# Kernel tuning notes

Hardware: AMD Instinct MI355X
Metric: run time of the kernel (lower is better)

Reference implementation:

```python
import jax, jax.numpy as jnp
import numpy as np

EPS = 1e-8


def _entropy_1d(p):
    # entropy() helper with input_as_probabilities=True on a 1-D tensor:
    # clamp to EPS, x*log(x), return -sum
    p_ = jnp.maximum(p, EPS)
    return -jnp.sum(p_ * jnp.log(p_))


def setup_inputs() -> dict:
    key = jax.random.key(0)
    k1, k2 = jax.random.split(key)
    b, n = 65536, 512
    anchors = jax.random.normal(k1, (b, n), dtype=jnp.float32)
    neighbors = jax.random.normal(k2, (b, n), dtype=jnp.float32)
    return {"anchors": anchors, "neighbors": neighbors}


def reference(anchors, neighbors):
    entropy_weight = 2.0
    b, n = anchors.shape

    anchors_prob = jax.nn.softmax(anchors, axis=1)      # [b, n]
    positives_prob = jax.nn.softmax(neighbors, axis=1)  # [b, n]

    # bmm of [b,1,n] x [b,n,1] -> row-wise dot product, shape [b]
    similarity = jnp.einsum('bn,bn->b', anchors_prob, positives_prob)

    # BCELoss(similarity, ones) = -mean(log(sim)); torch clamps log at -100
    consistency_loss = -jnp.mean(jnp.maximum(jnp.log(similarity), -100.0))

    lg_sim = jnp.log(similarity)

    entropy_loss = _entropy_1d(jnp.mean(anchors_prob, axis=0))

    # cross/second-order: dot of clamped sim with clamped log-sim
    second_order_loss = jnp.dot(jnp.maximum(similarity, EPS),
                                jnp.maximum(lg_sim, EPS))

    # np.tile(sim, n).reshape(n, b) then view(b, n, 1): equivalent to the
    # flat [b*n] tiled vector reshaped row-major to [b, n]
    tiled_sim = jnp.tile(similarity, n).reshape(b, n)
    third_order_entropy = jnp.einsum('bn,bn->b', anchors_prob, tiled_sim)
    lg_third = jnp.log(third_order_entropy)
    third_order_loss = jnp.dot(jnp.maximum(third_order_entropy, EPS),
                               jnp.maximum(lg_third, EPS)) / n

    third_weight = 0.5 / np.sqrt(n)
    diff_weight = 0.25 / n

    total_loss = (consistency_loss
                  - entropy_weight * entropy_loss
                  + diff_weight * second_order_loss
                  - third_weight * third_order_loss)
    return (total_loss, consistency_loss, entropy_loss,
            second_order_loss, third_order_loss)
```

## Files before the change

### kernel.cpp

```cpp
#include <hip/hip_runtime.h>
#include <math.h>

#define B_ROWS 65536
#define N_COLS 512
#define EPS 1e-8f
#define GRID1 2048


__global__ __launch_bounds__(256) void k_main(
        const float* __restrict__ A, const float* __restrict__ Bn,
        float* __restrict__ sim, float* __restrict__ colsum,
        float* __restrict__ acc) {
    __shared__ float cs[512];
    __shared__ float sred[8];
    const int t    = threadIdx.x;
    const int lane = t & 63;
    const int w    = t >> 6;
    const int s    = blockIdx.x & 127;
    const int kb   = (blockIdx.x >> 7) * 32 + w * 8;

    cs[t] = 0.f; cs[t + 256] = 0.f;

    float cacc[8];
#pragma unroll
    for (int k = 0; k < 8; ++k) cacc[k] = 0.f;
    float accLog = 0.f, accSim = 0.f;

#pragma unroll
    for (int batch = 0; batch < 2; ++batch) {
        int rows[4];
        float4 a0[4], a1[4], b0[4], b1[4];
#pragma unroll
        for (int q = 0; q < 4; ++q) {
            rows[q] = s + 128 * (kb + batch * 4 + q);
            const float* a = A  + (size_t)rows[q] * N_COLS;
            const float* b = Bn + (size_t)rows[q] * N_COLS;
            a0[q] = *(const float4*)(a + lane * 4);
            a1[q] = *(const float4*)(a + 256 + lane * 4);
            b0[q] = *(const float4*)(b + lane * 4);
            b1[q] = *(const float4*)(b + 256 + lane * 4);
        }
        float ea[4][8], sa[4], sb[4], dp[4];
#pragma unroll
        for (int q = 0; q < 4; ++q) {
            float av[8] = {a0[q].x, a0[q].y, a0[q].z, a0[q].w,
                           a1[q].x, a1[q].y, a1[q].z, a1[q].w};
            float bv[8] = {b0[q].x, b0[q].y, b0[q].z, b0[q].w,
                           b1[q].x, b1[q].y, b1[q].z, b1[q].w};
            float sA = 0.f, sB = 0.f, d = 0.f;
#pragma unroll
            for (int k = 0; k < 8; ++k) {
                float e = __expf(av[k]);
                float f = __expf(bv[k]);
                ea[q][k] = e;
                sA += e; sB += f; d += e * f;
            }
            sa[q] = sA; sb[q] = sB; dp[q] = d;
        }
#pragma unroll
        for (int m = 32; m >= 1; m >>= 1) {
#pragma unroll
            for (int q = 0; q < 4; ++q) {
                sa[q] += __shfl_xor(sa[q], m, 64);
                sb[q] += __shfl_xor(sb[q], m, 64);
                dp[q] += __shfl_xor(dp[q], m, 64);
            }
        }
#pragma unroll
        for (int q = 0; q < 4; ++q) {
            float inv_sa = 1.f / sa[q];
#pragma unroll
            for (int k = 0; k < 8; ++k) cacc[k] += ea[q][k] * inv_sa;
            if (lane == 0) {
                float sv = dp[q] * inv_sa * (1.f / sb[q]);
                sim[rows[q]] = sv;
                float lg = __logf(sv);
                accLog += fmaxf(lg, -100.f);
                accSim += fmaxf(sv, EPS);
            }
        }
    }

    if (lane == 0) { sred[w] = accLog; sred[4 + w] = accSim; }
    __syncthreads();
#pragma unroll
    for (int k = 0; k < 4; ++k) atomicAdd(&cs[lane * 4 + k], cacc[k]);
#pragma unroll
    for (int k = 0; k < 4; ++k) atomicAdd(&cs[256 + lane * 4 + k], cacc[4 + k]);
    __syncthreads();

    float* cdst = colsum + (size_t)s * 512;
    atomicAdd(&cdst[t], cs[t]);
    atomicAdd(&cdst[t + 256], cs[t + 256]);
    if (t == 0) atomicAdd(&acc[0], sred[0] + sred[1] + sred[2] + sred[3]);
    if (t == 1) atomicAdd(&acc[1], sred[4] + sred[5] + sred[6] + sred[7]);
}

__global__ __launch_bounds__(512) void k_final(
        const float* __restrict__ colsum, const float* __restrict__ sim,
        const float* __restrict__ acc, float* __restrict__ out) {
    __shared__ float red[16];
    const int t    = threadIdx.x;
    const int lane = t & 63;
    const int w    = t >> 6;

    float tot = 0.f, toe = 0.f;
#pragma unroll 4
    for (int s = 0; s < 128; ++s) {
        float c = colsum[s * 512 + t];
        tot += c;
        toe += c * sim[s * 512 + t];
    }
    float p   = fmaxf(tot * (1.f / B_ROWS), EPS);
    float ent = -p * __logf(p);

#pragma unroll
    for (int m = 32; m >= 1; m >>= 1) {
        ent += __shfl_xor(ent, m, 64);
        toe += __shfl_xor(toe, m, 64);
    }
    if (lane == 0) { red[w] = ent; red[8 + w] = toe; }
    __syncthreads();
    if (t == 0) {
        float entropy = 0.f, toeT = 0.f;
#pragma unroll
        for (int i = 0; i < 8; ++i) { entropy += red[i]; toeT += red[8 + i]; }
        float consistency = -acc[0] * (1.f / B_ROWS);
        float second      = acc[1] * EPS;
        float third       = toeT * EPS * (1.f / N_COLS);
        float third_weight = 0.5f / sqrtf((float)N_COLS);
        float diff_weight  = 0.25f / (float)N_COLS;
        float total = consistency - 2.0f * entropy + diff_weight * second
                      - third_weight * third;
        out[0] = total;
        out[1] = consistency;
        out[2] = entropy;
        out[3] = second;
        out[4] = third;
    }
}

extern "C" void kernel_launch(void* const* d_in, const int* in_sizes, int n_in,
                              void* d_out, int out_size, void* d_ws, size_t ws_size,
                              hipStream_t stream) {
    const float* anchors   = (const float*)d_in[0];
    const float* neighbors = (const float*)d_in[1];
    float* out = (float*)d_out;

    float* sim    = (float*)d_ws;
    float* colsum = sim + B_ROWS;
    float* acc    = colsum + 128 * 512;

    hipMemsetAsync(colsum, 0, (128 * 512 + 16) * sizeof(float), stream);

    k_main<<<dim3(GRID1), dim3(256), 0, stream>>>(
        anchors, neighbors, sim, colsum, acc);
    k_final<<<dim3(1), dim3(512), 0, stream>>>(colsum, sim, acc, out);
}
```

Measured before the change: 297.3 us.

## Software-pipeline row loads in main kernel and parallelize final reduction

The main kernel now walks its 8 rows one at a time in a non-unrolled loop and prefetches the next row's data while computing the current one. This replaces the earlier batched 4-row register loads, lowers register pressure, and adds a launch bound hint asking for higher occupancy. The single-block final reduction is split into a 64-block partial reduction kernel plus a tiny finisher kernel, which removes a serial 128-iteration loop but adds one extra launch and more atomics. Fewer rows in flight per wave could reduce memory-level parallelism.

Measured after the change: 328.9 us. +10.6%, slower.

```diff
diff --git a/kernel.cpp b/kernel.cpp
--- a/kernel.cpp
+++ b/kernel.cpp
@@ -7,12 +7,12 @@
 #define GRID1 2048
 
 
-__global__ __launch_bounds__(256) void k_main(
+__global__ __launch_bounds__(256, 8) void k_main(
         const float* __restrict__ A, const float* __restrict__ Bn,
         float* __restrict__ sim, float* __restrict__ colsum,
         float* __restrict__ acc) {
     __shared__ float cs[512];
-    __shared__ float sred[8];
+    __shared__ float sred[16];
     const int t    = threadIdx.x;
     const int lane = t & 63;
     const int w    = t >> 6;
@@ -26,62 +26,54 @@
     for (int k = 0; k < 8; ++k) cacc[k] = 0.f;
     float accLog = 0.f, accSim = 0.f;
 
+    size_t off = (size_t)(s + 128 * kb) * N_COLS + lane * 4;
+    float4 a0 = *(const float4*)(A  + off);
+    float4 a1 = *(const float4*)(A  + off + 256);
+    float4 b0 = *(const float4*)(Bn + off);
+    float4 b1 = *(const float4*)(Bn + off + 256);
+
+#pragma unroll 1
+    for (int r = 0; r < 8; ++r) {
+        float4 na0, na1, nb0, nb1;
+        if (r < 7) {
+            size_t noff = off + (size_t)128 * N_COLS;
+            na0 = *(const float4*)(A  + noff);
+            na1 = *(const float4*)(A  + noff + 256);
+            nb0 = *(const float4*)(Bn + noff);
+            nb1 = *(const float4*)(Bn + noff + 256);
+        }
+
+        const float av[8] = {a0.x, a0.y, a0.z, a0.w, a1.x, a1.y, a1.z, a1.w};
+        const float bv[8] = {b0.x, b0.y, b0.z, b0.w, b1.x, b1.y, b1.z, b1.w};
+        float ea[8];
+        float sA = 0.f, sB = 0.f, d = 0.f;
 #pragma unroll
-    for (int batch = 0; batch < 2; ++batch) {
-        int rows[4];
-        float4 a0[4], a1[4], b0[4], b1[4];
-#pragma unroll
-        for (int q = 0; q < 4; ++q) {
-            rows[q] = s + 128 * (kb + batch * 4 + q);
-            const float* a = A  + (size_t)rows[q] * N_COLS;
-            const float* b = Bn + (size_t)rows[q] * N_COLS;
-            a0[q] = *(const float4*)(a + lane * 4);
-            a1[q] = *(const float4*)(a + 256 + lane * 4);
-            b0[q] = *(const float4*)(b + lane * 4);
-            b1[q] = *(const float4*)(b + 256 + lane * 4);
-        }
-        float ea[4][8], sa[4], sb[4], dp[4];
-#pragma unroll
-        for (int q = 0; q < 4; ++q) {
-            float av[8] = {a0[q].x, a0[q].y, a0[q].z, a0[q].w,
-                           a1[q].x, a1[q].y, a1[q].z, a1[q].w};
-            float bv[8] = {b0[q].x, b0[q].y, b0[q].z, b0[q].w,
-                           b1[q].x, b1[q].y, b1[q].z, b1[q].w};
-            float sA = 0.f, sB = 0.f, d = 0.f;
-#pragma unroll
-            for (int k = 0; k < 8; ++k) {
-                float e = __expf(av[k]);
-                float f = __expf(bv[k]);
-                ea[q][k] = e;
-                sA += e; sB += f; d += e * f;
-            }
-            sa[q] = sA; sb[q] = sB; dp[q] = d;
+        for (int k = 0; k < 8; ++k) {
+            float e = __expf(av[k]);
+            float f = __expf(bv[k]);
+            ea[k] = e;
+            sA += e; sB += f; d += e * f;
         }
 #pragma unroll
         for (int m = 32; m >= 1; m >>= 1) {
+            sA += __shfl_xor(sA, m, 64);
+            sB += __shfl_xor(sB, m, 64);
+            d  += __shfl_xor(d,  m, 64);
+        }
+        float inv_sa = 1.f / sA;
 #pragma unroll
-            for (int q = 0; q < 4; ++q) {
-                sa[q] += __shfl_xor(sa[q], m, 64);
-                sb[q] += __shfl_xor(sb[q], m, 64);
-                dp[q] += __shfl_xor(dp[q], m, 64);
-            }
+        for (int k = 0; k < 8; ++k) cacc[k] += ea[k] * inv_sa;
+        if (lane == 0) {
+            float sv = d * inv_sa * (1.f / sB);
+            sim[s + 128 * (kb + r)] = sv;
+            accLog += fmaxf(__logf(sv), -100.f);
+            accSim += fmaxf(sv, EPS);
         }
-#pragma unroll
-        for (int q = 0; q < 4; ++q) {
-            float inv_sa = 1.f / sa[q];
-#pragma unroll
-            for (int k = 0; k < 8; ++k) cacc[k] += ea[q][k] * inv_sa;
-            if (lane == 0) {
-                float sv = dp[q] * inv_sa * (1.f / sb[q]);
-                sim[rows[q]] = sv;
-                float lg = __logf(sv);
-                accLog += fmaxf(lg, -100.f);
-                accSim += fmaxf(sv, EPS);
-            }
-        }
+        if (r < 7) { a0 = na0; a1 = na1; b0 = nb0; b1 = nb1; }
+        off += (size_t)128 * N_COLS;
     }
 
-    if (lane == 0) { sred[w] = accLog; sred[4 + w] = accSim; }
+    if (lane == 0) { sred[w] = accLog; sred[8 + w] = accSim; }
     __syncthreads();
 #pragma unroll
     for (int k = 0; k < 4; ++k) atomicAdd(&cs[lane * 4 + k], cacc[k]);
@@ -93,46 +85,56 @@
     atomicAdd(&cdst[t], cs[t]);
     atomicAdd(&cdst[t + 256], cs[t + 256]);
     if (t == 0) atomicAdd(&acc[0], sred[0] + sred[1] + sred[2] + sred[3]);
-    if (t == 1) atomicAdd(&acc[1], sred[4] + sred[5] + sred[6] + sred[7]);
+    if (t == 1) atomicAdd(&acc[1], sred[8] + sred[9] + sred[10] + sred[11]);
 }
 
-__global__ __launch_bounds__(512) void k_final(
+__global__ __launch_bounds__(512) void k_red(
         const float* __restrict__ colsum, const float* __restrict__ sim,
-        const float* __restrict__ acc, float* __restrict__ out) {
-    __shared__ float red[16];
-    const int t    = threadIdx.x;
-    const int lane = t & 63;
-    const int w    = t >> 6;
-
+        float* __restrict__ colTot, float* __restrict__ acc) {
+    __shared__ float red[8];
+    const int t = threadIdx.x, lane = t & 63, w = t >> 6;
+    const int s0 = blockIdx.x * 2;
     float tot = 0.f, toe = 0.f;
-#pragma unroll 4
-    for (int s = 0; s < 128; ++s) {
-        float c = colsum[s * 512 + t];
+#pragma unroll
+    for (int k = 0; k < 2; ++k) {
+        int idx = (s0 + k) * 512 + t;
+        float c = colsum[idx];
         tot += c;
-        toe += c * sim[s * 512 + t];
+        toe += c * sim[idx];
     }
-    float p   = fmaxf(tot * (1.f / B_ROWS), EPS);
-    float ent = -p * __logf(p);
-
+    atomicAdd(&colTot[t], tot);
 #pragma unroll
-    for (int m = 32; m >= 1; m >>= 1) {
-        ent += __shfl_xor(ent, m, 64);
-        toe += __shfl_xor(toe, m, 64);
-    }
-    if (lane == 0) { red[w] = ent; red[8 + w] = toe; }
+    for (int m = 32; m >= 1; m >>= 1) toe += __shfl_xor(toe, m, 64);
+    if (lane == 0) red[w] = toe;
     __syncthreads();
     if (t == 0) {
-        float entropy = 0.f, toeT = 0.f;
+        float tt = red[0] + red[1] + red[2] + red[3]
+                 + red[4] + red[5] + red[6] + red[7];
+        atomicAdd(&acc[2], tt);
+    }
+}
+
+__global__ __launch_bounds__(512) void k_fin(
+        const float* __restrict__ colTot, const float* __restrict__ acc,
+        float* __restrict__ out) {
+    __shared__ float red[8];
+    const int t = threadIdx.x, lane = t & 63, w = t >> 6;
+    float p   = fmaxf(colTot[t] * (1.f / B_ROWS), EPS);
+    float ent = -p * __logf(p);
 #pragma unroll
-        for (int i = 0; i < 8; ++i) { entropy += red[i]; toeT += red[8 + i]; }
+    for (int m = 32; m >= 1; m >>= 1) ent += __shfl_xor(ent, m, 64);
+    if (lane == 0) red[w] = ent;
+    __syncthreads();
+    if (t == 0) {
+        float entropy = red[0] + red[1] + red[2] + red[3]
+                      + red[4] + red[5] + red[6] + red[7];
         float consistency = -acc[0] * (1.f / B_ROWS);
         float second      = acc[1] * EPS;
-        float third       = toeT * EPS * (1.f / N_COLS);
+        float third       = acc[2] * EPS * (1.f / N_COLS);
         float third_weight = 0.5f / sqrtf((float)N_COLS);
         float diff_weight  = 0.25f / (float)N_COLS;
-        float total = consistency - 2.0f * entropy + diff_weight * second
-                      - third_weight * third;
-        out[0] = total;
+        out[0] = consistency - 2.0f * entropy + diff_weight * second
+                 - third_weight * third;
         out[1] = consistency;
         out[2] = entropy;
         out[3] = second;
@@ -149,11 +151,13 @@
 
     float* sim    = (float*)d_ws;
     float* colsum = sim + B_ROWS;
-    float* acc    = colsum + 128 * 512;
+    float* colTot = colsum + 128 * 512;
+    float* acc    = colTot + 512;
 
-    hipMemsetAsync(colsum, 0, (128 * 512 + 16) * sizeof(float), stream);
+    hipMemsetAsync(colsum, 0, (128 * 512 + 512 + 16) * sizeof(float), stream);
 
     k_main<<<dim3(GRID1), dim3(256), 0, stream>>>(
         anchors, neighbors, sim, colsum, acc);
-    k_final<<<dim3(1), dim3(512), 0, stream>>>(colsum, sim, acc, out);
+    k_red<<<dim3(64), dim3(512), 0, stream>>>(colsum, sim, colTot, acc);
+    k_fin<<<dim3(1), dim3(512), 0, stream>>>(colTot, acc, out);
 }
```
